# Performance work log

Measured on AMD Instinct MI355X. Metric: run time of the kernel, lower is better.

The kernel has to match this reference:

```python
import jax, jax.numpy as jnp
import numpy as np

H = 1024        # hidden_size
NH = 16         # num_attention_heads
DH = H // NH    # head dim = 64
I = 4096        # intermediate_size
E = 8           # moe_num_experts
B, S = 2, 2048
EPS = 1e-12


def _ln(x, g, b):
    mu = jnp.mean(x, axis=-1, keepdims=True)
    var = jnp.mean(jnp.square(x - mu), axis=-1, keepdims=True)
    return (x - mu) * jax.lax.rsqrt(var + EPS) * g + b


def setup_inputs() -> dict:
    key = jax.random.key(0)
    ks = jax.random.split(key, 16)
    std = 0.02
    p = {
        "hidden_states": jax.random.normal(ks[0], (B, S, H), jnp.float32),
        "Wq": jax.random.normal(ks[1], (H, H), jnp.float32) * std,
        "bq": jnp.zeros((H,), jnp.float32),
        "Wk": jax.random.normal(ks[2], (H, H), jnp.float32) * std,
        "bk": jnp.zeros((H,), jnp.float32),
        "Wv": jax.random.normal(ks[3], (H, H), jnp.float32) * std,
        "bv": jnp.zeros((H,), jnp.float32),
        "Wao": jax.random.normal(ks[4], (H, H), jnp.float32) * std,
        "bao": jnp.zeros((H,), jnp.float32),
        "ln1_g": jnp.ones((H,), jnp.float32),
        "ln1_b": jnp.zeros((H,), jnp.float32),
        "router_w": jax.random.normal(ks[5], (H, E), jnp.float32) * std,
        "We": jax.random.normal(ks[6], (E, H, I), jnp.float32) * std,
        "be": jnp.zeros((E, I), jnp.float32),
        "Wo": jax.random.normal(ks[7], (I, H), jnp.float32) * std,
        "bo": jnp.zeros((H,), jnp.float32),
        "ln2_g": jnp.ones((H,), jnp.float32),
        "ln2_b": jnp.zeros((H,), jnp.float32),
    }
    return p


def reference(hidden_states, Wq, bq, Wk, bk, Wv, bv, Wao, bao, ln1_g, ln1_b,
              router_w, We, be, Wo, bo, ln2_g, ln2_b):
    x = hidden_states  # [B,S,H]

    def heads(t):  # [B,S,H] -> [B,NH,S,DH]
        return t.reshape(B, S, NH, DH).transpose(0, 2, 1, 3)

    q = heads(x @ Wq + bq)
    k = heads(x @ Wk + bk)
    v = heads(x @ Wv + bv)
    scores = jnp.einsum("bhqd,bhkd->bhqk", q, k) / jnp.sqrt(jnp.float32(DH))
    probs = jax.nn.softmax(scores, axis=-1)
    ctx = jnp.einsum("bhqk,bhkd->bhqd", probs, v)
    ctx = ctx.transpose(0, 2, 1, 3).reshape(B, S, H)
    attn_out = _ln(ctx @ Wao + bao + x, ln1_g, ln1_b)  # BertSelfOutput

    # ---- MoE FFN: top-1 routing, per-expert GELU MLP, shared output proj ----
    flat = attn_out.reshape(-1, H)              # [N,H]
    logits = flat @ router_w                    # [N,E]
    idx = jnp.argmax(logits, axis=-1)           # top-1 of softmax == argmax of logits
    inter = jnp.zeros((flat.shape[0], I), flat.dtype)
    for e in range(E):  # small fixed expert count
        h_e = jax.nn.gelu(flat @ We[e] + be[e], approximate=False)
        inter = jnp.where((idx == e)[:, None], h_e, inter)
    inter = inter.reshape(B, S, I)
    out = _ln(inter @ Wo + bo + attn_out, ln2_g, ln2_b)  # BertOutput
    return out
```

## Files before the change

kernel.cpp:

```cpp
#include <hip/hip_runtime.h>
#include <hip/hip_bf16.h>
#include <cstdint>

#define H_  1024
#define NH_ 16
#define DH_ 64
#define I_  4096
#define E_  8
#define B_  2
#define S_  2048
#define N_  4096
#define QKVLD 3072
#define LN_EPS 1e-12f

typedef __attribute__((ext_vector_type(4))) float f4;
typedef __attribute__((ext_vector_type(8))) short s8v;
typedef unsigned int u32;

__device__ __forceinline__ float bf2f(unsigned short u) {
  union { unsigned int i; float f; } c; c.i = ((unsigned int)u) << 16; return c.f;
}
__device__ __forceinline__ unsigned short f2bf(float f) {
  __hip_bfloat16 h = __float2bfloat16(f);
  return *reinterpret_cast<unsigned short*>(&h);
}
__device__ __forceinline__ u32 pack_bf2(float a, float b) {
  return (u32)f2bf(a) | ((u32)f2bf(b) << 16);
}
__device__ __forceinline__ float gelu_f(float x) {
  return 0.5f * x * (1.0f + erff(x * 0.70710678118f));
}
__device__ __forceinline__ void gload16(const void* g, void* l) {
  __builtin_amdgcn_global_load_lds(
      (const __attribute__((address_space(1))) void*)g,
      (__attribute__((address_space(3))) void*)l, 16, 0, 0);
}

__global__ __launch_bounds__(256) void cvt_bf16_kernel(
    const float* __restrict__ in, ushort* __restrict__ out, int n8)
{
  const int t = blockIdx.x * 256 + threadIdx.x;
  if (t >= n8) return;
  const f4 x0 = *(const f4*)(in + (size_t)t * 8);
  const f4 x1 = *(const f4*)(in + (size_t)t * 8 + 4);
  s8v o;
#pragma unroll
  for (int j = 0; j < 4; ++j) { o[j] = (short)f2bf(x0[j]); o[4 + j] = (short)f2bf(x1[j]); }
  *(s8v*)(out + (size_t)t * 8) = o;
}

__global__ __launch_bounds__(256) void transpose_cvt_kernel(
    const float* __restrict__ in, ushort* __restrict__ out, int R, int C)
{
  __shared__ float tile[32][33];
  const size_t zo = (size_t)blockIdx.z * R * C;
  const int bx = blockIdx.x << 5, by = blockIdx.y << 5;
  const int tx = threadIdx.x & 31, ty = threadIdx.x >> 5;
  const float* ip = in + zo + (size_t)by * C + bx;
#pragma unroll
  for (int i = 0; i < 4; ++i)
    tile[ty + 8 * i][tx] = ip[(size_t)(ty + 8 * i) * C + tx];
  __syncthreads();
  ushort* op = out + zo + (size_t)bx * R + by;
#pragma unroll
  for (int i = 0; i < 4; ++i)
    op[(size_t)(ty + 8 * i) * R + tx] = f2bf(tile[tx][ty + 8 * i]);
}

__global__ void concat3_kernel(const float* a, const float* b, const float* c,
                               float* __restrict__ o)
{
  const int t = blockIdx.x * 256 + threadIdx.x;
  if (t < 1024) o[t] = a[t];
  else if (t < 2048) o[t] = b[t - 1024];
  else o[t] = c[t - 2048];
}

template <bool BF16OUT, int KSPLIT>
__global__ __launch_bounds__(256, 3) void gemm_mfma_kernel(
    const ushort* __restrict__ A, const ushort* __restrict__ Bt,
    const float* __restrict__ bias, void* __restrict__ Cout,
    const int M, const int N, const int K)
{
  __shared__ __align__(16) ushort Asm[2][4][128][8];
  __shared__ __align__(16) ushort Bsm[2][4][128][8];
  const int tid = threadIdx.x;
  const int w = tid >> 6, l = tid & 63;
  const int lq = l & 15, g = l >> 4;
  const int wm = w >> 1, wn = w & 1;
  const int nbx = N >> 7;
  const int nwg = nbx * (M >> 7);
  int id = blockIdx.y * nbx + blockIdx.x;
  id = (id & 7) * (nwg >> 3) + (id >> 3);
  const int m0 = (id / nbx) << 7, n0 = (id % nbx) << 7;
  const int Kspan = K / KSPLIT;
  const int kbase = (KSPLIT > 1) ? blockIdx.z * Kspan : 0;

  const ushort* a0 = A + (size_t)(m0 + l) * K + kbase + (w << 3);
  const ushort* a1 = a0 + (size_t)64 * K;
  const ushort* b0 = Bt + (size_t)(n0 + l) * K + kbase + (w << 3);
  const ushort* b1 = b0 + (size_t)64 * K;

  f4 acc[4][4] = {};
  const int nt = Kspan >> 5;
  gload16(a0, &Asm[0][w][0][0]);  gload16(a1, &Asm[0][w][64][0]);
  gload16(b0, &Bsm[0][w][0][0]);  gload16(b1, &Bsm[0][w][64][0]);
  __syncthreads();
  int cur = 0;
  for (int t = 0; t < nt; ++t) {
    if (t + 1 < nt) {
      const int kt = (t + 1) << 5;
      gload16(a0 + kt, &Asm[cur ^ 1][w][0][0]);
      gload16(a1 + kt, &Asm[cur ^ 1][w][64][0]);
      gload16(b0 + kt, &Bsm[cur ^ 1][w][0][0]);
      gload16(b1 + kt, &Bsm[cur ^ 1][w][64][0]);
    }
    s8v af[4], bfv[4];
#pragma unroll
    for (int mi = 0; mi < 4; ++mi)
      af[mi] = *(const s8v*)&Asm[cur][g][(wm << 6) + (mi << 4) + lq][0];
#pragma unroll
    for (int ni = 0; ni < 4; ++ni)
      bfv[ni] = *(const s8v*)&Bsm[cur][g][(wn << 6) + (ni << 4) + lq][0];
#pragma unroll
    for (int mi = 0; mi < 4; ++mi)
#pragma unroll
      for (int ni = 0; ni < 4; ++ni)
        acc[mi][ni] = __builtin_amdgcn_mfma_f32_16x16x32_bf16(af[mi], bfv[ni], acc[mi][ni], 0, 0, 0);
    __syncthreads();
    cur ^= 1;
  }
  float* outf = (float*)Cout + (size_t)blockIdx.z * M * N;
#pragma unroll
  for (int ni = 0; ni < 4; ++ni) {
    const int col = n0 + (wn << 6) + (ni << 4) + lq;
    const float bs = (KSPLIT == 1 || blockIdx.z == 0) ? bias[col] : 0.f;
#pragma unroll
    for (int mi = 0; mi < 4; ++mi) {
      const int row = m0 + (wm << 6) + (mi << 4) + (g << 2);
#pragma unroll
      for (int r = 0; r < 4; ++r) {
        const float val = acc[mi][ni][r] + bs;
        if constexpr (BF16OUT) ((ushort*)Cout)[(size_t)(row + r) * N + col] = f2bf(val);
        else                   outf[(size_t)(row + r) * N + col] = val;
      }
    }
  }
}

__global__ __launch_bounds__(256, 3) void moe_mfma_kernel(
    const ushort* __restrict__ X, const ushort* __restrict__ WeT,
    const float* __restrict__ be, const int* __restrict__ lists,
    const int* __restrict__ offs, const int* __restrict__ cnt,
    const int* __restrict__ tb, ushort* __restrict__ inter)
{
  __shared__ __align__(16) ushort Asm[2][4][128][8];
  __shared__ __align__(16) ushort Bsm[2][4][128][8];
  __shared__ int tokL[128];
  const int by = blockIdx.y;
  if (by >= tb[E_]) return;
  int e = 0;
#pragma unroll
  for (int t = 1; t < E_; ++t) if (by >= tb[t]) e = t;
  const int rt = by - tb[e];
  const int base = offs[e] + (rt << 7);
  const int nrows = cnt[e] - (rt << 7);
  const int tid = threadIdx.x;
  if (tid < 128) tokL[tid] = (tid < nrows) ? lists[base + tid] : -1;
  const int w = tid >> 6, l = tid & 63;
  const int lq = l & 15, g = l >> 4;
  const int wm = w >> 1, wn = w & 1;
  const int n0 = blockIdx.x << 7;
  const int t0 = (l < nrows) ? lists[base + l] : lists[base];
  const int t1 = (64 + l < nrows) ? lists[base + 64 + l] : lists[base];
  const ushort* a0 = X + (size_t)t0 * H_ + (w << 3);
  const ushort* a1 = X + (size_t)t1 * H_ + (w << 3);
  const ushort* Wp = WeT + (size_t)e * I_ * H_;
  const ushort* b0 = Wp + (size_t)(n0 + l) * H_ + (w << 3);
  const ushort* b1 = b0 + (size_t)64 * H_;

  f4 acc[4][4] = {};
  gload16(a0, &Asm[0][w][0][0]);  gload16(a1, &Asm[0][w][64][0]);
  gload16(b0, &Bsm[0][w][0][0]);  gload16(b1, &Bsm[0][w][64][0]);
  __syncthreads();
  int cur = 0;
  for (int t = 0; t < 32; ++t) {
    if (t + 1 < 32) {
      const int kt = (t + 1) << 5;
      gload16(a0 + kt, &Asm[cur ^ 1][w][0][0]);
      gload16(a1 + kt, &Asm[cur ^ 1][w][64][0]);
      gload16(b0 + kt, &Bsm[cur ^ 1][w][0][0]);
      gload16(b1 + kt, &Bsm[cur ^ 1][w][64][0]);
    }
    s8v af[4], bfv[4];
#pragma unroll
    for (int mi = 0; mi < 4; ++mi)
      af[mi] = *(const s8v*)&Asm[cur][g][(wm << 6) + (mi << 4) + lq][0];
#pragma unroll
    for (int ni = 0; ni < 4; ++ni)
      bfv[ni] = *(const s8v*)&Bsm[cur][g][(wn << 6) + (ni << 4) + lq][0];
#pragma unroll
    for (int mi = 0; mi < 4; ++mi)
#pragma unroll
      for (int ni = 0; ni < 4; ++ni)
        acc[mi][ni] = __builtin_amdgcn_mfma_f32_16x16x32_bf16(af[mi], bfv[ni], acc[mi][ni], 0, 0, 0);
    __syncthreads();
    cur ^= 1;
  }
#pragma unroll
  for (int ni = 0; ni < 4; ++ni) {
    const int col = n0 + (wn << 6) + (ni << 4) + lq;
    const float bs = be[(size_t)e * I_ + col];
#pragma unroll
    for (int mi = 0; mi < 4; ++mi) {
      const int rloc = (wm << 6) + (mi << 4) + (g << 2);
#pragma unroll
      for (int r = 0; r < 4; ++r) {
        const int tok = tokL[rloc + r];
        if (tok >= 0)
          inter[(size_t)tok * I_ + col] = f2bf(gelu_f(acc[mi][ni][r] + bs));
      }
    }
  }
}

__global__ __launch_bounds__(256) void attn_mfma_kernel(
    const ushort* __restrict__ qkv, ushort* __restrict__ ctx)
{
  __shared__ __align__(16) ushort Ks[64 * 72];
  __shared__ __align__(16) ushort Vt[64 * 72];
  __shared__ __align__(16) ushort Ps[4][16 * 72];
  const int bid0 = blockIdx.x;
  const int bid  = ((bid0 & 7) << 7) + (bid0 >> 3);
  const int bh = bid >> 5, qt = bid & 31;
  const int b = bh >> 4, h = bh & 15;
  const int tid = threadIdx.x, w = tid >> 6, l = tid & 63;
  const int lq = l & 15, g = l >> 4;
  const size_t bS = (size_t)b * S_;
  const ushort* qb = qkv + bS * QKVLD + h * DH_;
  const ushort* kb = qb + 1024;
  const ushort* vb = qb + 2048;

  s8v qf0, qf1;
  {
    const ushort* qp = qb + (size_t)(qt * 64 + w * 16 + lq) * QKVLD;
    qf0 = *(const s8v*)(qp + (g << 3));
    qf1 = *(const s8v*)(qp + 32 + (g << 3));
  }

  f4 o0 = {0,0,0,0}, o1 = {0,0,0,0}, o2 = {0,0,0,0}, o3 = {0,0,0,0};
  float mrun = -3.0e38f, lrun = 0.f;

  const int skey = tid >> 2;
  const int sd   = (tid & 3) << 4;

  for (int kt = 0; kt < 32; ++kt) {
    __syncthreads();
    {
      const ushort* kp = kb + (size_t)(kt * 64 + skey) * QKVLD + sd;
      *(s8v*)&Ks[skey * 72 + sd]     = *(const s8v*)(kp);
      *(s8v*)&Ks[skey * 72 + sd + 8] = *(const s8v*)(kp + 8);
      const ushort* vp = vb + (size_t)(kt * 64 + skey) * QKVLD + sd;
      const s8v v0 = *(const s8v*)(vp);
      const s8v v1 = *(const s8v*)(vp + 8);
#pragma unroll
      for (int ii = 0; ii < 8; ++ii) {
        Vt[(sd + ii) * 72 + skey]     = v0[ii];
        Vt[(sd + 8 + ii) * 72 + skey] = v1[ii];
      }
    }
    __syncthreads();

    float s[16];
#pragma unroll
    for (int st = 0; st < 4; ++st) {
      f4 acc = {0, 0, 0, 0};
      const s8v ka0 = *(const s8v*)&Ks[(st * 16 + lq) * 72 + (g << 3)];
      const s8v ka1 = *(const s8v*)&Ks[(st * 16 + lq) * 72 + 32 + (g << 3)];
      acc = __builtin_amdgcn_mfma_f32_16x16x32_bf16(ka0, qf0, acc, 0, 0, 0);
      acc = __builtin_amdgcn_mfma_f32_16x16x32_bf16(ka1, qf1, acc, 0, 0, 0);
      s[st * 4 + 0] = acc[0] * 0.125f; s[st * 4 + 1] = acc[1] * 0.125f;
      s[st * 4 + 2] = acc[2] * 0.125f; s[st * 4 + 3] = acc[3] * 0.125f;
    }

    float tmax = s[0];
#pragma unroll
    for (int i = 1; i < 16; ++i) tmax = fmaxf(tmax, s[i]);
    tmax = fmaxf(tmax, __shfl_xor(tmax, 16));
    tmax = fmaxf(tmax, __shfl_xor(tmax, 32));
    const float mnew  = fmaxf(mrun, tmax);
    const float alpha = __expf(mrun - mnew);
    float psum = 0.f;
#pragma unroll
    for (int i = 0; i < 16; ++i) { s[i] = __expf(s[i] - mnew); psum += s[i]; }
    psum += __shfl_xor(psum, 16); psum += __shfl_xor(psum, 32);
    lrun = lrun * alpha + psum; mrun = mnew;

    f4 av;
    av[0] = __shfl(alpha, g * 4 + 0); av[1] = __shfl(alpha, g * 4 + 1);
    av[2] = __shfl(alpha, g * 4 + 2); av[3] = __shfl(alpha, g * 4 + 3);
    o0 *= av; o1 *= av; o2 *= av; o3 *= av;

    {
      ushort* pw = &Ps[w][lq * 72];
#pragma unroll
      for (int st = 0; st < 4; ++st) {
        *(u32*)&pw[st * 16 + g * 4 + 0] = pack_bf2(s[st * 4 + 0], s[st * 4 + 1]);
        *(u32*)&pw[st * 16 + g * 4 + 2] = pack_bf2(s[st * 4 + 2], s[st * 4 + 3]);
      }
    }
    asm volatile("s_waitcnt lgkmcnt(0)" ::: "memory");
    __builtin_amdgcn_sched_barrier(0);

#pragma unroll
    for (int ks = 0; ks < 2; ++ks) {
      const int kof = ks * 32 + (g << 3);
      const s8v pa = *(const s8v*)&Ps[w][lq * 72 + kof];
      const s8v v0 = *(const s8v*)&Vt[( 0 + lq) * 72 + kof];
      const s8v v1 = *(const s8v*)&Vt[(16 + lq) * 72 + kof];
      const s8v v2 = *(const s8v*)&Vt[(32 + lq) * 72 + kof];
      const s8v v3 = *(const s8v*)&Vt[(48 + lq) * 72 + kof];
      o0 = __builtin_amdgcn_mfma_f32_16x16x32_bf16(pa, v0, o0, 0, 0, 0);
      o1 = __builtin_amdgcn_mfma_f32_16x16x32_bf16(pa, v1, o1, 0, 0, 0);
      o2 = __builtin_amdgcn_mfma_f32_16x16x32_bf16(pa, v2, o2, 0, 0, 0);
      o3 = __builtin_amdgcn_mfma_f32_16x16x32_bf16(pa, v3, o3, 0, 0, 0);
    }
  }

  const float inv = 1.f / lrun;
#pragma unroll
  for (int r = 0; r < 4; ++r) {
    const float li = __shfl(inv, g * 4 + r);
    ushort* op = ctx + (bS + (size_t)(qt * 64 + w * 16 + g * 4 + r)) * H_ + h * DH_ + lq;
    op[0]  = f2bf(o0[r] * li);
    op[16] = f2bf(o1[r] * li);
    op[32] = f2bf(o2[r] * li);
    op[48] = f2bf(o3[r] * li);
  }
}

template <int P>
__global__ __launch_bounds__(256) void add_ln_kernel(
    const float* __restrict__ a, const float* __restrict__ r,
    const float* __restrict__ g, const float* __restrict__ bta,
    float* __restrict__ out, ushort* __restrict__ ob)
{
  const int row = blockIdx.x, tid = threadIdx.x;
  const size_t base = (size_t)row * H_;
  const float4 xr = *(const float4*)(r + base + (tid << 2));
  float4 x = xr;
#pragma unroll
  for (int pp = 0; pp < P; ++pp) {
    const float4 xa = *(const float4*)(a + (size_t)pp * N_ * H_ + base + (tid << 2));
    x.x += xa.x; x.y += xa.y; x.z += xa.z; x.w += xa.w;
  }
  float s  = x.x + x.y + x.z + x.w;
  float ss = x.x * x.x + x.y * x.y + x.z * x.z + x.w * x.w;
#pragma unroll
  for (int off = 1; off < 64; off <<= 1) { s += __shfl_xor(s, off); ss += __shfl_xor(ss, off); }
  __shared__ float red[8];
  const int w = tid >> 6, ln = tid & 63;
  if (ln == 0) { red[w] = s; red[4 + w] = ss; }
  __syncthreads();
  const float S  = red[0] + red[1] + red[2] + red[3];
  const float SS = red[4] + red[5] + red[6] + red[7];
  const float mu  = S * (1.f / 1024.f);
  const float var = fmaxf(SS * (1.f / 1024.f) - mu * mu, 0.f);
  const float inv = rsqrtf(var + LN_EPS);
  const float4 gg = *(const float4*)&g[tid << 2];
  const float4 bb = *(const float4*)&bta[tid << 2];
  float4 y;
  y.x = (x.x - mu) * inv * gg.x + bb.x;
  y.y = (x.y - mu) * inv * gg.y + bb.y;
  y.z = (x.z - mu) * inv * gg.z + bb.z;
  y.w = (x.w - mu) * inv * gg.w + bb.w;
  *(float4*)&out[base + (tid << 2)] = y;
  if (ob) {
    ushort4 u;
    u.x = f2bf(y.x); u.y = f2bf(y.y); u.z = f2bf(y.z); u.w = f2bf(y.w);
    *(ushort4*)&ob[base + (tid << 2)] = u;
  }
}

__global__ __launch_bounds__(64) void router_kernel(
    const float* __restrict__ x, const float* __restrict__ rw,
    int* __restrict__ idx, int* __restrict__ cnt)
{
  const int t = blockIdx.x, lane = threadIdx.x;
  float acc[8] = {0.f};
  for (int c = 0; c < H_; c += 64) {
    const float xv = x[(size_t)t * H_ + c + lane];
    const float* wr = rw + (size_t)(c + lane) * E_;
    const float4 w0 = *(const float4*)wr;
    const float4 w1 = *(const float4*)(wr + 4);
    acc[0] += xv * w0.x; acc[1] += xv * w0.y; acc[2] += xv * w0.z; acc[3] += xv * w0.w;
    acc[4] += xv * w1.x; acc[5] += xv * w1.y; acc[6] += xv * w1.z; acc[7] += xv * w1.w;
  }
#pragma unroll
  for (int e = 0; e < E_; ++e) {
    float s = acc[e];
#pragma unroll
    for (int off = 1; off < 64; off <<= 1) s += __shfl_xor(s, off);
    acc[e] = s;
  }
  if (lane == 0) {
    int be_ = 0; float bv = acc[0];
#pragma unroll
    for (int e = 1; e < E_; ++e) if (acc[e] > bv) { bv = acc[e]; be_ = e; }
    idx[t] = be_;
    atomicAdd(&cnt[be_], 1);
  }
}

__global__ void init_kernel(int* cnt) { if (threadIdx.x < E_) cnt[threadIdx.x] = 0; }

__global__ void scan_kernel(const int* __restrict__ cnt, int* __restrict__ offs,
                            int* __restrict__ cursor, int* __restrict__ tb)
{
  int o = 0, tt = 0;
  for (int e = 0; e < E_; ++e) {
    offs[e] = o; cursor[e] = o; tb[e] = tt;
    o += cnt[e]; tt += (cnt[e] + 127) >> 7;
  }
  tb[E_] = tt;
}

__global__ __launch_bounds__(256) void scatter_kernel(
    const int* __restrict__ idx, int* __restrict__ cursor, int* __restrict__ lists)
{
  const int t = blockIdx.x * 256 + threadIdx.x;
  if (t < N_) {
    const int e = idx[t];
    const int p = atomicAdd(&cursor[e], 1);
    lists[p] = t;
  }
}

extern "C" void kernel_launch(void* const* d_in, const int* in_sizes, int n_in,
                              void* d_out, int out_size, void* d_ws, size_t ws_size,
                              hipStream_t stream) {
  const float* x   = (const float*)d_in[0];
  const float* Wq  = (const float*)d_in[1];
  const float* bq  = (const float*)d_in[2];
  const float* Wk  = (const float*)d_in[3];
  const float* bk  = (const float*)d_in[4];
  const float* Wv  = (const float*)d_in[5];
  const float* bv  = (const float*)d_in[6];
  const float* Wao = (const float*)d_in[7];
  const float* bao = (const float*)d_in[8];
  const float* g1  = (const float*)d_in[9];
  const float* b1  = (const float*)d_in[10];
  const float* rw  = (const float*)d_in[11];
  const float* We  = (const float*)d_in[12];
  const float* be  = (const float*)d_in[13];
  const float* Wo  = (const float*)d_in[14];
  const float* bo  = (const float*)d_in[15];
  const float* g2  = (const float*)d_in[16];
  const float* b2  = (const float*)d_in[17];
  float* out = (float*)d_out;

  char* p = (char*)d_ws;
  int* idx    = (int*)p; p += (size_t)N_ * 4;
  int* cnt    = (int*)p; p += 8 * 4;
  int* offs   = (int*)p; p += 8 * 4;
  int* cursor = (int*)p; p += 8 * 4;
  int* tb     = (int*)p; p += 16 * 4;
  int* lists  = (int*)p; p += (size_t)N_ * 4;
  p = (char*)(((uintptr_t)p + 255) & ~(uintptr_t)255);
  const size_t NH = (size_t)N_ * H_;
  ushort* xb     = (ushort*)p; p += NH * 2;
  ushort* qkvb   = (ushort*)p;
  float*  woPart = (float*)p;  p += (size_t)N_ * QKVLD * 2;
  ushort* ctxb   = (ushort*)p; p += NH * 2;
  float*  attn   = (float*)p;  p += NH * 4;
  ushort* attnb  = (ushort*)p; p += NH * 2;
  ushort* interb = (ushort*)p;
  float*  aoPart = (float*)p;  p += (size_t)N_ * I_ * 2;
  ushort* WqkvT  = (ushort*)p; p += (size_t)QKVLD * H_ * 2;
  ushort* WaoT   = (ushort*)p; p += (size_t)H_ * H_ * 2;
  ushort* WoT    = (ushort*)p; p += (size_t)H_ * I_ * 2;
  ushort* WeT    = (ushort*)p; p += (size_t)E_ * I_ * H_ * 2;
  float*  bqkv   = (float*)p;  p += QKVLD * 4;

  const dim3 blk(256);

  init_kernel<<<1, 64, 0, stream>>>(cnt);
  cvt_bf16_kernel<<<(N_ * H_ / 8 + 255) / 256, blk, 0, stream>>>(x, xb, N_ * H_ / 8);
  concat3_kernel<<<QKVLD / 256, blk, 0, stream>>>(bq, bk, bv, bqkv);
  transpose_cvt_kernel<<<dim3(32, 32, 1), blk, 0, stream>>>(Wq, WqkvT, H_, H_);
  transpose_cvt_kernel<<<dim3(32, 32, 1), blk, 0, stream>>>(Wk, WqkvT + (size_t)1024 * H_, H_, H_);
  transpose_cvt_kernel<<<dim3(32, 32, 1), blk, 0, stream>>>(Wv, WqkvT + (size_t)2048 * H_, H_, H_);
  transpose_cvt_kernel<<<dim3(32, 32, 1), blk, 0, stream>>>(Wao, WaoT, H_, H_);
  transpose_cvt_kernel<<<dim3(32, 128, 1), blk, 0, stream>>>(Wo, WoT, I_, H_);
  transpose_cvt_kernel<<<dim3(128, 32, 8), blk, 0, stream>>>(We, WeT, H_, I_);

  gemm_mfma_kernel<true, 1><<<dim3(QKVLD / 128, N_ / 128), blk, 0, stream>>>(
      xb, WqkvT, bqkv, qkvb, N_, QKVLD, H_);
  attn_mfma_kernel<<<1024, blk, 0, stream>>>(qkvb, ctxb);
  gemm_mfma_kernel<false, 2><<<dim3(H_ / 128, N_ / 128, 2), blk, 0, stream>>>(
      ctxb, WaoT, bao, aoPart, N_, H_, H_);
  add_ln_kernel<2><<<N_, blk, 0, stream>>>(aoPart, x, g1, b1, attn, attnb);
  router_kernel<<<N_, 64, 0, stream>>>(attn, rw, idx, cnt);
  scan_kernel<<<1, 1, 0, stream>>>(cnt, offs, cursor, tb);
  scatter_kernel<<<N_ / 256, blk, 0, stream>>>(idx, cursor, lists);
  moe_mfma_kernel<<<dim3(I_ / 128, N_ / 128 + E_), blk, 0, stream>>>(
      attnb, WeT, be, lists, offs, cnt, tb, interb);
  gemm_mfma_kernel<false, 2><<<dim3(H_ / 128, N_ / 128, 2), blk, 0, stream>>>(
      interb, WoT, bo, woPart, N_, H_, I_);
  add_ln_kernel<2><<<N_, blk, 0, stream>>>(woPart, attn, g2, b2, out, (ushort*)nullptr);
}
```

Baseline: 545.9 us.

## Pre-gather MoE tokens contiguously and stage bf16 epilogues through LDS for vector stores

Adds a gather kernel that copies routed token rows into expert-sorted contiguous order, reusing the xb buffer, so the MoE GEMM loads its A operand from sequential rows instead of indirect per-token addresses. The bf16-output GEMM and MoE epilogues now stage each 16-row tile in shared memory and write 16-byte vectors per row rather than scattered 2-byte stores. The cost is an extra kernel launch plus one read and one write of the activations, and an extra barrier in the MoE kernel.

```diff
diff --git a/kernel.cpp b/kernel.cpp
--- a/kernel.cpp
+++ b/kernel.cpp
@@ -74,6 +74,16 @@
   if (t < 1024) o[t] = a[t];
   else if (t < 2048) o[t] = b[t - 1024];
   else o[t] = c[t - 2048];
+}
+
+__global__ __launch_bounds__(256) void gather_kernel(
+    const ushort* __restrict__ X, const int* __restrict__ lists,
+    ushort* __restrict__ Xg)
+{
+  const int r = (blockIdx.x << 1) + (threadIdx.x >> 7);
+  const int c = (threadIdx.x & 127) << 3;
+  const int tok = lists[r];
+  *(s8v*)&Xg[(size_t)r * H_ + c] = *(const s8v*)&X[(size_t)tok * H_ + c];
 }
 
 template <bool BF16OUT, int KSPLIT>
@@ -130,26 +140,45 @@
     __syncthreads();
     cur ^= 1;
   }
-  float* outf = (float*)Cout + (size_t)blockIdx.z * M * N;
-#pragma unroll
-  for (int ni = 0; ni < 4; ++ni) {
-    const int col = n0 + (wn << 6) + (ni << 4) + lq;
-    const float bs = (KSPLIT == 1 || blockIdx.z == 0) ? bias[col] : 0.f;
+  if constexpr (BF16OUT) {
+    ushort* st = (ushort*)Asm + (size_t)w * (16 * 72);
+    float bs[4];
+#pragma unroll
+    for (int ni = 0; ni < 4; ++ni) bs[ni] = bias[n0 + (wn << 6) + (ni << 4) + lq];
 #pragma unroll
     for (int mi = 0; mi < 4; ++mi) {
-      const int row = m0 + (wm << 6) + (mi << 4) + (g << 2);
-#pragma unroll
-      for (int r = 0; r < 4; ++r) {
-        const float val = acc[mi][ni][r] + bs;
-        if constexpr (BF16OUT) ((ushort*)Cout)[(size_t)(row + r) * N + col] = f2bf(val);
-        else                   outf[(size_t)(row + r) * N + col] = val;
+#pragma unroll
+      for (int ni = 0; ni < 4; ++ni)
+#pragma unroll
+        for (int r = 0; r < 4; ++r)
+          st[((g << 2) + r) * 72 + (ni << 4) + lq] = f2bf(acc[mi][ni][r] + bs[ni]);
+#pragma unroll
+      for (int q2 = 0; q2 < 2; ++q2) {
+        const int r16 = l & 15, ch = (l >> 4) + (q2 << 2);
+        const s8v vv = *(const s8v*)&st[r16 * 72 + (ch << 3)];
+        *(s8v*)&((ushort*)Cout)[(size_t)(m0 + (wm << 6) + (mi << 4) + r16) * N
+                                + n0 + (wn << 6) + (ch << 3)] = vv;
       }
     }
+  } else {
+    float* outf = (float*)Cout + (size_t)blockIdx.z * M * N;
+#pragma unroll
+    for (int ni = 0; ni < 4; ++ni) {
+      const int col = n0 + (wn << 6) + (ni << 4) + lq;
+      const float bs = (KSPLIT == 1 || blockIdx.z == 0) ? bias[col] : 0.f;
+#pragma unroll
+      for (int mi = 0; mi < 4; ++mi) {
+        const int row = m0 + (wm << 6) + (mi << 4) + (g << 2);
+#pragma unroll
+        for (int r = 0; r < 4; ++r)
+          outf[(size_t)(row + r) * N + col] = acc[mi][ni][r] + bs;
+      }
+    }
   }
 }
 
 __global__ __launch_bounds__(256, 3) void moe_mfma_kernel(
-    const ushort* __restrict__ X, const ushort* __restrict__ WeT,
+    const ushort* __restrict__ Xg, const ushort* __restrict__ WeT,
     const float* __restrict__ be, const int* __restrict__ lists,
     const int* __restrict__ offs, const int* __restrict__ cnt,
     const int* __restrict__ tb, ushort* __restrict__ inter)
@@ -167,14 +196,15 @@
   const int nrows = cnt[e] - (rt << 7);
   const int tid = threadIdx.x;
   if (tid < 128) tokL[tid] = (tid < nrows) ? lists[base + tid] : -1;
+  __syncthreads();
   const int w = tid >> 6, l = tid & 63;
   const int lq = l & 15, g = l >> 4;
   const int wm = w >> 1, wn = w & 1;
   const int n0 = blockIdx.x << 7;
-  const int t0 = (l < nrows) ? lists[base + l] : lists[base];
-  const int t1 = (64 + l < nrows) ? lists[base + 64 + l] : lists[base];
-  const ushort* a0 = X + (size_t)t0 * H_ + (w << 3);
-  const ushort* a1 = X + (size_t)t1 * H_ + (w << 3);
+  const int r0 = min(base + l, N_ - 1);
+  const int r1 = min(base + 64 + l, N_ - 1);
+  const ushort* a0 = Xg + (size_t)r0 * H_ + (w << 3);
+  const ushort* a1 = Xg + (size_t)r1 * H_ + (w << 3);
   const ushort* Wp = WeT + (size_t)e * I_ * H_;
   const ushort* b0 = Wp + (size_t)(n0 + l) * H_ + (w << 3);
   const ushort* b1 = b0 + (size_t)64 * H_;
@@ -207,18 +237,26 @@
     __syncthreads();
     cur ^= 1;
   }
-#pragma unroll
-  for (int ni = 0; ni < 4; ++ni) {
-    const int col = n0 + (wn << 6) + (ni << 4) + lq;
-    const float bs = be[(size_t)e * I_ + col];
+  {
+    ushort* st = (ushort*)Asm + (size_t)w * (16 * 72);
+    float bs[4];
+#pragma unroll
+    for (int ni = 0; ni < 4; ++ni) bs[ni] = be[(size_t)e * I_ + n0 + (wn << 6) + (ni << 4) + lq];
 #pragma unroll
     for (int mi = 0; mi < 4; ++mi) {
-      const int rloc = (wm << 6) + (mi << 4) + (g << 2);
-#pragma unroll
-      for (int r = 0; r < 4; ++r) {
-        const int tok = tokL[rloc + r];
-        if (tok >= 0)
-          inter[(size_t)tok * I_ + col] = f2bf(gelu_f(acc[mi][ni][r] + bs));
+#pragma unroll
+      for (int ni = 0; ni < 4; ++ni)
+#pragma unroll
+        for (int r = 0; r < 4; ++r)
+          st[((g << 2) + r) * 72 + (ni << 4) + lq] = f2bf(gelu_f(acc[mi][ni][r] + bs[ni]));
+#pragma unroll
+      for (int q2 = 0; q2 < 2; ++q2) {
+        const int r16 = l & 15, ch = (l >> 4) + (q2 << 2);
+        const int tok = tokL[(wm << 6) + (mi << 4) + r16];
+        if (tok >= 0) {
+          const s8v vv = *(const s8v*)&st[r16 * 72 + (ch << 3)];
+          *(s8v*)&inter[(size_t)tok * I_ + n0 + (wn << 6) + (ch << 3)] = vv;
+        }
       }
     }
   }
@@ -481,6 +519,7 @@
   ushort* WoT    = (ushort*)p; p += (size_t)H_ * I_ * 2;
   ushort* WeT    = (ushort*)p; p += (size_t)E_ * I_ * H_ * 2;
   float*  bqkv   = (float*)p;  p += QKVLD * 4;
+  ushort* Xg     = xb;
 
   const dim3 blk(256);
 
@@ -503,8 +542,9 @@
   router_kernel<<<N_, 64, 0, stream>>>(attn, rw, idx, cnt);
   scan_kernel<<<1, 1, 0, stream>>>(cnt, offs, cursor, tb);
   scatter_kernel<<<N_ / 256, blk, 0, stream>>>(idx, cursor, lists);
+  gather_kernel<<<N_ / 2, blk, 0, stream>>>(attnb, lists, Xg);
   moe_mfma_kernel<<<dim3(I_ / 128, N_ / 128 + E_), blk, 0, stream>>>(
-      attnb, WeT, be, lists, offs, cnt, tb, interb);
+      Xg, WeT, be, lists, offs, cnt, tb, interb);
   gemm_mfma_kernel<false, 2><<<dim3(H_ / 128, N_ / 128, 2), blk, 0, stream>>>(
       interb, WoT, bo, woPart, N_, H_, I_);
   add_ln_kernel<2><<<N_, blk, 0, stream>>>(woPart, attn, g2, b2, out, (ushort*)nullptr);
```

New measurement: 538.3 us. Within noise of the previous version (-1.4%).
